# Optimization experiments

Measured on AMD Instinct MI355X. Metric: run time of the kernel, lower is better.

## Reference

```python
import jax, jax.numpy as jnp
import numpy as np
from jax import lax

B, T, N_MELS = 8, 4096, 26
W_FRAMES = 32          # window_frames
CONV_CH, CONV_K = 64, 5
SE_MID = CONV_CH // 4  # se_ratio=4 on feature_dim=conv_channels
H1, H2 = 256, 128      # hidden_dims
SHORT_W, SHORT_H = 8, 128
OUT_CH = 2             # downbeat=True


def setup_inputs() -> dict:
    key = jax.random.key(0)
    ks = jax.random.split(key, 16)
    s = lambda *sh: 1.0 / np.sqrt(sh[0])
    return {
        "x": jax.random.normal(ks[0], (B, T, N_MELS), jnp.float32),
        # conv1d: kernel stored (K, in, out) for NWC/WIO conv
        "conv_w": jax.random.normal(ks[1], (CONV_K, N_MELS, CONV_CH), jnp.float32) * 0.1,
        "conv_b": jax.random.normal(ks[2], (CONV_CH,), jnp.float32) * 0.1,
        # SE on feature_dim=CONV_CH
        "se_w1": jax.random.normal(ks[3], (CONV_CH, SE_MID), jnp.float32) * s(CONV_CH),
        "se_b1": jnp.zeros((SE_MID,), jnp.float32),
        "se_w2": jax.random.normal(ks[4], (SE_MID, CONV_CH), jnp.float32) * s(SE_MID),
        "se_b2": jnp.zeros((CONV_CH,), jnp.float32),
        # long backbone: (W_FRAMES*CONV_CH) -> H1 -> H2
        "w1": jax.random.normal(ks[5], (W_FRAMES * CONV_CH, H1), jnp.float32) * s(W_FRAMES * CONV_CH),
        "b1": jnp.zeros((H1,), jnp.float32),
        "w2": jax.random.normal(ks[6], (H1, H2), jnp.float32) * s(H1),
        "b2": jnp.zeros((H2,), jnp.float32),
        # short backbone: (SHORT_W*CONV_CH) -> SHORT_H
        "sw": jax.random.normal(ks[7], (SHORT_W * CONV_CH, SHORT_H), jnp.float32) * s(SHORT_W * CONV_CH),
        "sb": jnp.zeros((SHORT_H,), jnp.float32),
        # output head: (H2 + SHORT_H) -> OUT_CH
        "wo": jax.random.normal(ks[8], (H2 + SHORT_H, OUT_CH), jnp.float32) * s(H2 + SHORT_H),
        "bo": jnp.zeros((OUT_CH,), jnp.float32),
    }


def reference(x, conv_w, conv_b, se_w1, se_b1, se_w2, se_b2,
              w1, b1, w2, b2, sw, sb, wo, bo):
    batch, time, _ = x.shape
    # 1) causal conv1d over full sequence (left-pad K-1), then ReLU
    xp = jnp.pad(x, ((0, 0), (CONV_K - 1, 0), (0, 0)))
    xc = lax.conv_general_dilated(xp, conv_w, window_strides=(1,),
                                  padding='VALID',
                                  dimension_numbers=('NWC', 'WIO', 'NWC'))
    xc = jax.nn.relu(xc + conv_b)                      # (B, T, F=CONV_CH)
    # 2) causal sliding-window unfold: windows[b,t,w,:] = padded[b, t+w, :]
    x_pad = jnp.pad(xc, ((0, 0), (W_FRAMES - 1, 0), (0, 0)))
    idx = jnp.arange(time)[:, None] + jnp.arange(W_FRAMES)[None, :]
    windows = x_pad[:, idx, :]                          # (B, T, W, F)
    # 3) SE channel attention (pool over window dim)
    s = windows.mean(axis=2)                            # (B, T, F)
    a = jax.nn.sigmoid(jax.nn.relu(s @ se_w1 + se_b1) @ se_w2 + se_b2)
    windows = windows * a[:, :, None, :]
    # 4) long backbone (dropout = identity in eval)
    flat_long = windows.reshape(batch, time, W_FRAMES * CONV_CH)
    h = jax.nn.relu(flat_long @ w1 + b1)
    h = jax.nn.relu(h @ w2 + b2)                        # (B, T, H2)
    # short path: last SHORT_W frames of the same SE-processed window
    flat_short = windows[:, :, -SHORT_W:, :].reshape(batch, time, SHORT_W * CONV_CH)
    h_short = jax.nn.relu(flat_short @ sw + sb)         # (B, T, SHORT_H)
    h = jnp.concatenate([h, h_short], axis=-1)
    # 5) output head
    return jax.nn.sigmoid(h @ wo + bo)                  # (B, T, OUT_CH)
```

## Files before the change

kernel.cpp:

```cpp
#include <hip/hip_runtime.h>

typedef _Float16 half_t;
typedef __attribute__((ext_vector_type(8))) _Float16 h8;
typedef __attribute__((ext_vector_type(2))) _Float16 h2v;
typedef __attribute__((ext_vector_type(4))) float f4;
typedef __attribute__((ext_vector_type(2))) float f2v;

__device__ __forceinline__ half_t to_h(float v) {
    v = fminf(fmaxf(v, -60000.f), 60000.f);
    return (half_t)v;
}

__global__ void pack_k(const float* __restrict__ w1, const float* __restrict__ w2,
                       const float* __restrict__ sw, const float* __restrict__ cw,
                       half_t* __restrict__ wsH) {
    int i = blockIdx.x * 256 + threadIdx.x;
    if (i < 65536) {
        int L = i & 63, nt = (i >> 6) & 15, kk = i >> 10;
        int k0 = kk * 32 + ((L >> 4) << 3), n = (nt << 4) + (L & 15);
        h8 v;
#pragma unroll
        for (int j = 0; j < 8; j++) v[j] = to_h(w1[(k0 + j) * 256 + n]);
        *(h8*)(wsH + ((((kk * 16 + nt) * 64 + L)) << 3)) = v;
    } else if (i < 69632) {
        int o = i - 65536;
        int L = o & 63, nt = (o >> 6) & 7, kk = o >> 9;
        int k0 = kk * 32 + ((L >> 4) << 3), n = (nt << 4) + (L & 15);
        h8 v;
#pragma unroll
        for (int j = 0; j < 8; j++) v[j] = to_h(w2[(k0 + j) * 128 + n]);
        *(h8*)(wsH + 524288 + ((((kk * 8 + nt) * 64 + L)) << 3)) = v;
    } else if (i < 77824) {
        int o = i - 69632;
        int L = o & 63, nt = (o >> 6) & 7, kk = o >> 9;
        int k0 = kk * 32 + ((L >> 4) << 3), n = (nt << 4) + (L & 15);
        h8 v;
#pragma unroll
        for (int j = 0; j < 8; j++) v[j] = to_h(sw[(k0 + j) * 128 + n]);
        *(h8*)(wsH + 557056 + ((((kk * 8 + nt) * 64 + L)) << 3)) = v;
    } else if (i < 86144) {
        int o = i - 77824;
        int c = o & 63, rest = o >> 6;
        int k = rest / 26, ci = rest - k * 26;
        int ip = ci >> 1, r = ci & 1;
        wsH[622592 + ((k * 13 + ip) * 64 + c) * 2 + r] = to_h(cw[o]);
    }
}

#define XCS 72
#define ALS 72
#define Y1S 264
#define SLS 68
#define HLS 20

#define MFMA16(a, b, c) __builtin_amdgcn_mfma_f32_16x16x32_f16(a, b, c, 0, 0, 0)

__global__ __launch_bounds__(512, 4) void beat_main(
    const float* __restrict__ x,
    const float* __restrict__ conv_b,
    const float* __restrict__ se_w1, const float* __restrict__ se_b1,
    const float* __restrict__ se_w2, const float* __restrict__ se_b2,
    const float* __restrict__ b1, const float* __restrict__ b2,
    const float* __restrict__ sb,
    const float* __restrict__ wo, const float* __restrict__ bo,
    const half_t* __restrict__ w1p, const half_t* __restrict__ w2p,
    const half_t* __restrict__ swp, const half_t* __restrict__ cwp,
    float* __restrict__ out) {

    __shared__ __align__(16) char smem[58752];
    half_t* xcL = (half_t*)smem;
    half_t* aL  = (half_t*)(smem + 13696);
    char*   U   = smem + 22912;
    half_t* xLh = (half_t*)U;
    float*  sLf = (float*)U;
    float*  hidL= (float*)(U + 17408);
    half_t* y1L = (half_t*)U;
    float*  woL = (float*)(smem + 56704);

    const int tid = threadIdx.x;
    const int bi = blockIdx.x;
    const int b = bi >> 6;
    const int t0 = (bi & 63) << 6;
    const int lane = tid & 63, wv = tid >> 6;
    const int quad = lane >> 4, rl = lane & 15;
    const int mg = wv >> 2;
    const int ng = wv & 3;
    const int nq = wv & 3;

    if (tid < 256) ((f2v*)woL)[tid] = ((const f2v*)wo)[tid];
    for (int idx = tid; idx < 99 * 13; idx += 512) {
        int fi = idx / 13, ip = idx - fi * 13;
        int tx = t0 - 35 + fi;
        h2v v;
        if (tx >= 0) {
            const float* xp = x + ((size_t)(b * 4096 + tx)) * 26 + 2 * ip;
            v[0] = to_h(xp[0]); v[1] = to_h(xp[1]);
        } else { v[0] = (_Float16)0.f; v[1] = (_Float16)0.f; }
        *(h2v*)(xLh + fi * 28 + 2 * ip) = v;
    }
    __syncthreads();

    {
        int c = tid & 63, f0 = tid >> 6;
        h2v cwr[65];
        const h2v* cwg = (const h2v*)cwp;
#pragma unroll
        for (int p = 0; p < 65; p++) cwr[p] = cwg[p * 64 + c];
        float bias = conv_b[c];
        for (int f = f0; f < 95; f += 8) {
            int t = t0 - 31 + f;
            float r0 = 0.f;
            if (t >= 0) {
                h2v accp; accp[0] = (_Float16)0.f; accp[1] = (_Float16)0.f;
#pragma unroll
                for (int k = 0; k < 5; k++)
#pragma unroll
                    for (int ip = 0; ip < 13; ip++) {
                        h2v xp = *(const h2v*)(xLh + (f + k) * 28 + 2 * ip);
                        accp += xp * cwr[k * 13 + ip];
                    }
                r0 = fmaxf((float)accp[0] + (float)accp[1] + bias, 0.f);
            }
            xcL[f * XCS + c] = to_h(r0);
        }
    }
    __syncthreads();

    {
        int c = tid & 63, mb = tid >> 6;
        float run = 0.f;
#pragma unroll 8
        for (int w = 0; w < 32; w++) run += (float)xcL[(mb + w) * XCS + c];
        sLf[mb * SLS + c] = run * (1.f / 32.f);
        for (int m = mb + 8; m < 64; m += 8) {
#pragma unroll
            for (int d = 0; d < 8; d++) {
                run += (float)xcL[(m + 24 + d) * XCS + c];
                run -= (float)xcL[(m - 8 + d) * XCS + c];
            }
            sLf[m * SLS + c] = run * (1.f / 32.f);
        }
    }
    __syncthreads();

    {
        int m = tid >> 3, hh = (tid & 7) * 2;
        float acc0 = se_b1[hh], acc1 = se_b1[hh + 1];
        for (int c = 0; c < 64; c++) {
            float sv = sLf[m * SLS + c];
            f2v wq = *(const f2v*)(se_w1 + c * 16 + hh);
            acc0 += sv * wq[0]; acc1 += sv * wq[1];
        }
        hidL[m * HLS + hh] = fmaxf(acc0, 0.f);
        hidL[m * HLS + hh + 1] = fmaxf(acc1, 0.f);
    }
    __syncthreads();

    {
        int m = tid >> 3, c0 = (tid & 7) * 8;
        float av[8];
#pragma unroll
        for (int j = 0; j < 8; j++) av[j] = se_b2[c0 + j];
        for (int h = 0; h < 16; h++) {
            float hv = hidL[m * HLS + h];
            const f4* wv4 = (const f4*)(se_w2 + h * 64 + c0);
            f4 wq0 = wv4[0], wq1 = wv4[1];
#pragma unroll
            for (int j = 0; j < 4; j++) { av[j] += hv * wq0[j]; av[4 + j] += hv * wq1[j]; }
        }
#pragma unroll
        for (int j = 0; j < 8; j++) {
            float zz = fminf(fmaxf(av[j], -30.f), 30.f);
            float s = 1.f / (1.f + __expf(-zz));
            aL[m * ALS + c0 + j] = to_h(s);
        }
    }
    __syncthreads();

    {
        f4 acc[2][4];
#pragma unroll
        for (int mt = 0; mt < 2; mt++)
#pragma unroll
            for (int i = 0; i < 4; i++)
#pragma unroll
                for (int r = 0; r < 4; r++) acc[mt][i][r] = 0.f;
        const h8* w1v = (const h8*)w1p;
        const int fb = ng * 4;
        h8 bA[4], bB[4], bC[4], bD[4];
#pragma unroll
        for (int i = 0; i < 4; i++) bA[i] = w1v[(fb + i) * 64 + lane];
#pragma unroll
        for (int i = 0; i < 4; i++) bB[i] = w1v[(16 + fb + i) * 64 + lane];
#pragma unroll 2
        for (int kk = 0; kk < 64; kk += 2) {
            const int k2 = (kk + 2) & 63, k3 = (kk + 3) & 63;
#pragma unroll
            for (int i = 0; i < 4; i++) bC[i] = w1v[(k2 * 16 + fb + i) * 64 + lane];
#pragma unroll
            for (int i = 0; i < 4; i++) bD[i] = w1v[(k3 * 16 + fb + i) * 64 + lane];
            const int wf = kk >> 1;
            {
                const int c0 = quad * 8;
#pragma unroll
                for (int mt = 0; mt < 2; mt++) {
                    int m = mg * 32 + mt * 16 + rl;
                    h8 xv = *(const h8*)(xcL + (m + wf) * XCS + c0);
                    h8 av = *(const h8*)(aL + m * ALS + c0);
                    h8 af = xv * av;
#pragma unroll
                    for (int i = 0; i < 4; i++) acc[mt][i] = MFMA16(af, bA[i], acc[mt][i]);
                }
            }
            {
                const int c0 = 32 + quad * 8;
#pragma unroll
                for (int mt = 0; mt < 2; mt++) {
                    int m = mg * 32 + mt * 16 + rl;
                    h8 xv = *(const h8*)(xcL + (m + wf) * XCS + c0);
                    h8 av = *(const h8*)(aL + m * ALS + c0);
                    h8 af = xv * av;
#pragma unroll
                    for (int i = 0; i < 4; i++) acc[mt][i] = MFMA16(af, bB[i], acc[mt][i]);
                }
            }
#pragma unroll
            for (int i = 0; i < 4; i++) { bA[i] = bC[i]; bB[i] = bD[i]; }
        }
#pragma unroll
        for (int i = 0; i < 4; i++) {
            int n = ng * 64 + i * 16 + rl;
            float bb = b1[n];
#pragma unroll
            for (int mt = 0; mt < 2; mt++)
#pragma unroll
                for (int r = 0; r < 4; r++) {
                    int m = mg * 32 + mt * 16 + quad * 4 + r;
                    y1L[m * Y1S + n] = to_h(fmaxf(acc[mt][i][r] + bb, 0.f));
                }
        }
    }
    __syncthreads();

    f4 acc2[2][2];
#pragma unroll
    for (int mt = 0; mt < 2; mt++)
#pragma unroll
        for (int j = 0; j < 2; j++)
#pragma unroll
            for (int r = 0; r < 4; r++) acc2[mt][j][r] = 0.f;
    {
        const h8* w2v = (const h8*)w2p;
        const int fb2 = nq * 2;
        h8 c0f = w2v[(fb2 + 0) * 64 + lane];
        h8 c1f = w2v[(fb2 + 1) * 64 + lane];
#pragma unroll 2
        for (int kk = 0; kk < 8; kk++) {
            int kn = (kk + 1) & 7;
            h8 n0 = w2v[(kn * 8 + fb2 + 0) * 64 + lane];
            h8 n1 = w2v[(kn * 8 + fb2 + 1) * 64 + lane];
#pragma unroll
            for (int mt = 0; mt < 2; mt++) {
                h8 av = *(const h8*)(y1L + (mg * 32 + mt * 16 + rl) * Y1S + kk * 32 + quad * 8);
                acc2[mt][0] = MFMA16(av, c0f, acc2[mt][0]);
                acc2[mt][1] = MFMA16(av, c1f, acc2[mt][1]);
            }
            c0f = n0; c1f = n1;
        }
    }

    f4 accS[2][2];
#pragma unroll
    for (int mt = 0; mt < 2; mt++)
#pragma unroll
        for (int j = 0; j < 2; j++)
#pragma unroll
            for (int r = 0; r < 4; r++) accS[mt][j][r] = 0.f;
    {
        const h8* swv = (const h8*)swp;
        const int fb2 = nq * 2;
        h8 c0f = swv[(fb2 + 0) * 64 + lane];
        h8 c1f = swv[(fb2 + 1) * 64 + lane];
#pragma unroll 2
        for (int kk = 0; kk < 16; kk++) {
            int kn = (kk + 1) & 15;
            h8 n0 = swv[(kn * 8 + fb2 + 0) * 64 + lane];
            h8 n1 = swv[(kn * 8 + fb2 + 1) * 64 + lane];
            const int wf = 24 + (kk >> 1);
            const int c0 = ((kk & 1) << 5) + quad * 8;
#pragma unroll
            for (int mt = 0; mt < 2; mt++) {
                int m = mg * 32 + mt * 16 + rl;
                h8 xv = *(const h8*)(xcL + (m + wf) * XCS + c0);
                h8 av2 = *(const h8*)(aL + m * ALS + c0);
                h8 af = xv * av2;
                accS[mt][0] = MFMA16(af, c0f, accS[mt][0]);
                accS[mt][1] = MFMA16(af, c1f, accS[mt][1]);
            }
            c0f = n0; c1f = n1;
        }
    }
    __syncthreads();

    {
#pragma unroll
        for (int j = 0; j < 2; j++) {
            int n = nq * 32 + j * 16 + rl;
            float bb2 = b2[n], bbs = sb[n];
#pragma unroll
            for (int mt = 0; mt < 2; mt++)
#pragma unroll
                for (int r = 0; r < 4; r++) {
                    int m = mg * 32 + mt * 16 + quad * 4 + r;
                    y1L[m * Y1S + n]       = to_h(fmaxf(acc2[mt][j][r] + bb2, 0.f));
                    y1L[m * Y1S + 128 + n] = to_h(fmaxf(accS[mt][j][r] + bbs, 0.f));
                }
        }
    }
    __syncthreads();

    if (tid < 128) {
        int m = tid >> 1, o = tid & 1;
        float z = bo[o];
        const half_t* hrow = y1L + m * Y1S;
        for (int nb = 0; nb < 32; nb++) {
            h8 hv = *(const h8*)(hrow + nb * 8);
#pragma unroll
            for (int j = 0; j < 8; j++)
                z += (float)hv[j] * woL[(nb * 8 + j) * 2 + o];
        }
        z = fminf(fmaxf(z, -30.f), 30.f);
        float sg = 1.f / (1.f + __expf(-z));
        out[((size_t)(b * 4096 + t0 + m)) * 2 + o] = sg;
    }
}

extern "C" void kernel_launch(void* const* d_in, const int* in_sizes, int n_in,
                              void* d_out, int out_size, void* d_ws, size_t ws_size,
                              hipStream_t stream) {
    const float* x      = (const float*)d_in[0];
    const float* conv_w = (const float*)d_in[1];
    const float* conv_b = (const float*)d_in[2];
    const float* se_w1  = (const float*)d_in[3];
    const float* se_b1  = (const float*)d_in[4];
    const float* se_w2  = (const float*)d_in[5];
    const float* se_b2  = (const float*)d_in[6];
    const float* w1     = (const float*)d_in[7];
    const float* b1     = (const float*)d_in[8];
    const float* w2     = (const float*)d_in[9];
    const float* b2     = (const float*)d_in[10];
    const float* sw     = (const float*)d_in[11];
    const float* sb     = (const float*)d_in[12];
    const float* wo     = (const float*)d_in[13];
    const float* bo     = (const float*)d_in[14];
    half_t* wsH = (half_t*)d_ws;

    hipLaunchKernelGGL(pack_k, dim3(337), dim3(256), 0, stream, w1, w2, sw, conv_w, wsH);
    hipLaunchKernelGGL(beat_main, dim3(512), dim3(512), 0, stream,
                       x, conv_b, se_w1, se_b1, se_w2, se_b2, b1, b2, sb, wo, bo,
                       wsH, wsH + 524288, wsH + 557056, wsH + 622592,
                       (float*)d_out);
}
```

Measured before the change: 152.7 us.

## Split conv and SE attention into prep kernel, stream results into GEMM kernel

Moves the causal conv, sliding mean and SE attention out of the GEMM kernel into a prep kernel that also packs weights. The prep kernel handles 128-frame tiles, so the 31-frame halo conv is recomputed less often. It writes conv output and attention gates to global workspace in fp16. The GEMM kernel reloads these, keeps the gates in registers and uses less shared memory, which may raise occupancy. The cost is an extra global round trip for the intermediates and a serial dependency between the two launches.

```diff
diff --git a/kernel.cpp b/kernel.cpp
--- a/kernel.cpp
+++ b/kernel.cpp
@@ -11,71 +11,178 @@
     return (half_t)v;
 }
 
-__global__ void pack_k(const float* __restrict__ w1, const float* __restrict__ w2,
-                       const float* __restrict__ sw, const float* __restrict__ cw,
-                       half_t* __restrict__ wsH) {
-    int i = blockIdx.x * 256 + threadIdx.x;
-    if (i < 65536) {
-        int L = i & 63, nt = (i >> 6) & 15, kk = i >> 10;
-        int k0 = kk * 32 + ((L >> 4) << 3), n = (nt << 4) + (L & 15);
-        h8 v;
-#pragma unroll
-        for (int j = 0; j < 8; j++) v[j] = to_h(w1[(k0 + j) * 256 + n]);
-        *(h8*)(wsH + ((((kk * 16 + nt) * 64 + L)) << 3)) = v;
-    } else if (i < 69632) {
-        int o = i - 65536;
-        int L = o & 63, nt = (o >> 6) & 7, kk = o >> 9;
-        int k0 = kk * 32 + ((L >> 4) << 3), n = (nt << 4) + (L & 15);
-        h8 v;
-#pragma unroll
-        for (int j = 0; j < 8; j++) v[j] = to_h(w2[(k0 + j) * 128 + n]);
-        *(h8*)(wsH + 524288 + ((((kk * 8 + nt) * 64 + L)) << 3)) = v;
-    } else if (i < 77824) {
-        int o = i - 69632;
-        int L = o & 63, nt = (o >> 6) & 7, kk = o >> 9;
-        int k0 = kk * 32 + ((L >> 4) << 3), n = (nt << 4) + (L & 15);
-        h8 v;
-#pragma unroll
-        for (int j = 0; j < 8; j++) v[j] = to_h(sw[(k0 + j) * 128 + n]);
-        *(h8*)(wsH + 557056 + ((((kk * 8 + nt) * 64 + L)) << 3)) = v;
-    } else if (i < 86144) {
-        int o = i - 77824;
-        int c = o & 63, rest = o >> 6;
-        int k = rest / 26, ci = rest - k * 26;
-        int ip = ci >> 1, r = ci & 1;
-        wsH[622592 + ((k * 13 + ip) * 64 + c) * 2 + r] = to_h(cw[o]);
-    }
-}
-
-#define XCS 72
-#define ALS 72
-#define Y1S 264
-#define SLS 68
-#define HLS 20
-
-#define MFMA16(a, b, c) __builtin_amdgcn_mfma_f32_16x16x32_f16(a, b, c, 0, 0, 0)
-
-__global__ __launch_bounds__(512, 4) void beat_main(
-    const float* __restrict__ x,
+#define W2P_OFF 524288
+#define SWP_OFF 557056
+#define XCG_OFF 622592
+#define AG_OFF  2719744
+
+__global__ __launch_bounds__(512) void beat_prep(
+    const float* __restrict__ x, const float* __restrict__ conv_w,
     const float* __restrict__ conv_b,
     const float* __restrict__ se_w1, const float* __restrict__ se_b1,
     const float* __restrict__ se_w2, const float* __restrict__ se_b2,
+    const float* __restrict__ w1, const float* __restrict__ w2,
+    const float* __restrict__ sw,
+    half_t* __restrict__ wsH) {
+
+    const int bi = blockIdx.x;
+    const int tid = threadIdx.x;
+
+    if (bi >= 256) {
+        int j = (bi - 256) * 512 + tid;
+        if (j < 65536) {
+            int L = j & 63, nt = (j >> 6) & 15, kk = j >> 10;
+            int k0 = kk * 32 + ((L >> 4) << 3), n = (nt << 4) + (L & 15);
+            h8 v;
+#pragma unroll
+            for (int q = 0; q < 8; q++) v[q] = to_h(w1[(k0 + q) * 256 + n]);
+            *(h8*)(wsH + (((kk * 16 + nt) * 64 + L) << 3)) = v;
+        } else if (j < 69632) {
+            int o = j - 65536;
+            int L = o & 63, nt = (o >> 6) & 7, kk = o >> 9;
+            int k0 = kk * 32 + ((L >> 4) << 3), n = (nt << 4) + (L & 15);
+            h8 v;
+#pragma unroll
+            for (int q = 0; q < 8; q++) v[q] = to_h(w2[(k0 + q) * 128 + n]);
+            *(h8*)(wsH + W2P_OFF + (((kk * 8 + nt) * 64 + L) << 3)) = v;
+        } else {
+            int o = j - 69632;
+            int L = o & 63, nt = (o >> 6) & 7, kk = o >> 9;
+            int k0 = kk * 32 + ((L >> 4) << 3), n = (nt << 4) + (L & 15);
+            h8 v;
+#pragma unroll
+            for (int q = 0; q < 8; q++) v[q] = to_h(sw[(k0 + q) * 128 + n]);
+            *(h8*)(wsH + SWP_OFF + (((kk * 8 + nt) * 64 + L) << 3)) = v;
+        }
+        return;
+    }
+
+    __shared__ __align__(16) char smem[54560];
+    half_t* xLh  = (half_t*)smem;
+    half_t* xcA  = (half_t*)(smem + 9136);
+    float*  sLf  = (float*)(smem + 32032);
+    float*  hidL = (float*)(smem + 49440);
+    half_t* xc_g = wsH + XCG_OFF;
+    half_t* a_g  = wsH + AG_OFF;
+
+    const int b = bi >> 5;
+    const int t0a = (bi & 31) << 7;
+
+    for (int idx = tid; idx < 163 * 13; idx += 512) {
+        int fi = idx / 13, ip = idx - fi * 13;
+        int tx = t0a - 35 + fi;
+        h2v v;
+        if (tx >= 0) {
+            const float* xp = x + ((size_t)(b * 4096 + tx)) * 26 + 2 * ip;
+            v[0] = to_h(xp[0]); v[1] = to_h(xp[1]);
+        } else { v[0] = (_Float16)0.f; v[1] = (_Float16)0.f; }
+        *(h2v*)(xLh + fi * 28 + 2 * ip) = v;
+    }
+    __syncthreads();
+
+    {
+        int c = tid & 63, f0 = tid >> 6;
+        h2v cwr[65];
+#pragma unroll
+        for (int p = 0; p < 65; p++) {
+            int k = p / 13, ip = p - k * 13;
+            cwr[p][0] = to_h(conv_w[(k * 26 + 2 * ip) * 64 + c]);
+            cwr[p][1] = to_h(conv_w[(k * 26 + 2 * ip + 1) * 64 + c]);
+        }
+        float bias = conv_b[c];
+        for (int f = f0; f < 159; f += 8) {
+            int t = t0a + f - 31;
+            float r0 = 0.f;
+            if (t >= 0) {
+                h2v accp; accp[0] = (_Float16)0.f; accp[1] = (_Float16)0.f;
+#pragma unroll
+                for (int k = 0; k < 5; k++)
+#pragma unroll
+                    for (int ip = 0; ip < 13; ip++) {
+                        h2v xp = *(const h2v*)(xLh + (f + k) * 28 + 2 * ip);
+                        accp += xp * cwr[k * 13 + ip];
+                    }
+                r0 = fmaxf((float)accp[0] + (float)accp[1] + bias, 0.f);
+            }
+            half_t hv = to_h(r0);
+            xcA[f * 72 + c] = hv;
+            if (f >= 31) xc_g[((size_t)(b * 4096 + t)) * 64 + c] = hv;
+        }
+    }
+    __syncthreads();
+
+    for (int sub = 0; sub < 2; sub++) {
+        const int base = sub * 64;
+        {
+            int c = tid & 63, mb = tid >> 6;
+            float run = 0.f;
+#pragma unroll 8
+            for (int w = 0; w < 32; w++) run += (float)xcA[(base + mb + w) * 72 + c];
+            sLf[mb * 68 + c] = run * (1.f / 32.f);
+            for (int m = mb + 8; m < 64; m += 8) {
+#pragma unroll
+                for (int d = 0; d < 8; d++) {
+                    run += (float)xcA[(base + m + 24 + d) * 72 + c];
+                    run -= (float)xcA[(base + m - 8 + d) * 72 + c];
+                }
+                sLf[m * 68 + c] = run * (1.f / 32.f);
+            }
+        }
+        __syncthreads();
+        {
+            int m = tid >> 3, hh = (tid & 7) * 2;
+            float acc0 = se_b1[hh], acc1 = se_b1[hh + 1];
+            for (int c = 0; c < 64; c++) {
+                float sv = sLf[m * 68 + c];
+                f2v wq = *(const f2v*)(se_w1 + c * 16 + hh);
+                acc0 += sv * wq[0]; acc1 += sv * wq[1];
+            }
+            hidL[m * 20 + hh] = fmaxf(acc0, 0.f);
+            hidL[m * 20 + hh + 1] = fmaxf(acc1, 0.f);
+        }
+        __syncthreads();
+        {
+            int m = tid >> 3, c0 = (tid & 7) * 8;
+            float av[8];
+#pragma unroll
+            for (int q = 0; q < 8; q++) av[q] = se_b2[c0 + q];
+            for (int h = 0; h < 16; h++) {
+                float hv = hidL[m * 20 + h];
+                const f4* wv4 = (const f4*)(se_w2 + h * 64 + c0);
+                f4 wq0 = wv4[0], wq1 = wv4[1];
+#pragma unroll
+                for (int q = 0; q < 4; q++) { av[q] += hv * wq0[q]; av[4 + q] += hv * wq1[q]; }
+            }
+            h8 ov;
+#pragma unroll
+            for (int q = 0; q < 8; q++) {
+                float zz = fminf(fmaxf(av[q], -30.f), 30.f);
+                ov[q] = to_h(1.f / (1.f + __expf(-zz)));
+            }
+            *(h8*)(a_g + ((size_t)(b * 4096 + t0a + base + m)) * 64 + c0) = ov;
+        }
+        __syncthreads();
+    }
+}
+
+#define XCS 72
+#define Y1S 264
+
+#define MFMA16(a, b, c) __builtin_amdgcn_mfma_f32_16x16x32_f16(a, b, c, 0, 0, 0)
+
+__global__ __launch_bounds__(512, 4) void beat_gemm(
     const float* __restrict__ b1, const float* __restrict__ b2,
     const float* __restrict__ sb,
     const float* __restrict__ wo, const float* __restrict__ bo,
     const half_t* __restrict__ w1p, const half_t* __restrict__ w2p,
-    const half_t* __restrict__ swp, const half_t* __restrict__ cwp,
+    const half_t* __restrict__ swp,
+    const half_t* __restrict__ xc_g, const half_t* __restrict__ a_g,
     float* __restrict__ out) {
 
-    __shared__ __align__(16) char smem[58752];
+    __shared__ __align__(16) char smem[49536];
     half_t* xcL = (half_t*)smem;
-    half_t* aL  = (half_t*)(smem + 13696);
-    char*   U   = smem + 22912;
-    half_t* xLh = (half_t*)U;
-    float*  sLf = (float*)U;
-    float*  hidL= (float*)(U + 17408);
-    half_t* y1L = (half_t*)U;
-    float*  woL = (float*)(smem + 56704);
+    half_t* y1L = (half_t*)(smem + 13696);
+    float*  woL = (float*)(smem + 47488);
 
     const int tid = threadIdx.x;
     const int bi = blockIdx.x;
@@ -88,93 +195,23 @@
     const int nq = wv & 3;
 
     if (tid < 256) ((f2v*)woL)[tid] = ((const f2v*)wo)[tid];
-    for (int idx = tid; idx < 99 * 13; idx += 512) {
-        int fi = idx / 13, ip = idx - fi * 13;
-        int tx = t0 - 35 + fi;
-        h2v v;
-        if (tx >= 0) {
-            const float* xp = x + ((size_t)(b * 4096 + tx)) * 26 + 2 * ip;
-            v[0] = to_h(xp[0]); v[1] = to_h(xp[1]);
-        } else { v[0] = (_Float16)0.f; v[1] = (_Float16)0.f; }
-        *(h2v*)(xLh + fi * 28 + 2 * ip) = v;
-    }
-    __syncthreads();
-
-    {
-        int c = tid & 63, f0 = tid >> 6;
-        h2v cwr[65];
-        const h2v* cwg = (const h2v*)cwp;
-#pragma unroll
-        for (int p = 0; p < 65; p++) cwr[p] = cwg[p * 64 + c];
-        float bias = conv_b[c];
-        for (int f = f0; f < 95; f += 8) {
-            int t = t0 - 31 + f;
-            float r0 = 0.f;
-            if (t >= 0) {
-                h2v accp; accp[0] = (_Float16)0.f; accp[1] = (_Float16)0.f;
-#pragma unroll
-                for (int k = 0; k < 5; k++)
-#pragma unroll
-                    for (int ip = 0; ip < 13; ip++) {
-                        h2v xp = *(const h2v*)(xLh + (f + k) * 28 + 2 * ip);
-                        accp += xp * cwr[k * 13 + ip];
-                    }
-                r0 = fmaxf((float)accp[0] + (float)accp[1] + bias, 0.f);
-            }
-            xcL[f * XCS + c] = to_h(r0);
-        }
-    }
-    __syncthreads();
-
-    {
-        int c = tid & 63, mb = tid >> 6;
-        float run = 0.f;
-#pragma unroll 8
-        for (int w = 0; w < 32; w++) run += (float)xcL[(mb + w) * XCS + c];
-        sLf[mb * SLS + c] = run * (1.f / 32.f);
-        for (int m = mb + 8; m < 64; m += 8) {
-#pragma unroll
-            for (int d = 0; d < 8; d++) {
-                run += (float)xcL[(m + 24 + d) * XCS + c];
-                run -= (float)xcL[(m - 8 + d) * XCS + c];
-            }
-            sLf[m * SLS + c] = run * (1.f / 32.f);
-        }
-    }
-    __syncthreads();
-
-    {
-        int m = tid >> 3, hh = (tid & 7) * 2;
-        float acc0 = se_b1[hh], acc1 = se_b1[hh + 1];
-        for (int c = 0; c < 64; c++) {
-            float sv = sLf[m * SLS + c];
-            f2v wq = *(const f2v*)(se_w1 + c * 16 + hh);
-            acc0 += sv * wq[0]; acc1 += sv * wq[1];
-        }
-        hidL[m * HLS + hh] = fmaxf(acc0, 0.f);
-        hidL[m * HLS + hh + 1] = fmaxf(acc1, 0.f);
-    }
-    __syncthreads();
-
-    {
-        int m = tid >> 3, c0 = (tid & 7) * 8;
-        float av[8];
-#pragma unroll
-        for (int j = 0; j < 8; j++) av[j] = se_b2[c0 + j];
-        for (int h = 0; h < 16; h++) {
-            float hv = hidL[m * HLS + h];
-            const f4* wv4 = (const f4*)(se_w2 + h * 64 + c0);
-            f4 wq0 = wv4[0], wq1 = wv4[1];
-#pragma unroll
-            for (int j = 0; j < 4; j++) { av[j] += hv * wq0[j]; av[4 + j] += hv * wq1[j]; }
-        }
-#pragma unroll
-        for (int j = 0; j < 8; j++) {
-            float zz = fminf(fmaxf(av[j], -30.f), 30.f);
-            float s = 1.f / (1.f + __expf(-zz));
-            aL[m * ALS + c0 + j] = to_h(s);
-        }
-    }
+    for (int idx = tid; idx < 95 * 8; idx += 512) {
+        int fi = idx >> 3, jp = idx & 7;
+        int t = t0 - 31 + fi;
+        h8 v;
+        if (t >= 0) v = *(const h8*)(xc_g + ((size_t)(b * 4096 + t)) * 64 + jp * 8);
+        else {
+#pragma unroll
+            for (int q = 0; q < 8; q++) v[q] = (_Float16)0.f;
+        }
+        *(h8*)(xcL + fi * XCS + jp * 8) = v;
+    }
+    h8 avr[2][2];
+#pragma unroll
+    for (int mt = 0; mt < 2; mt++)
+#pragma unroll
+        for (int p = 0; p < 2; p++)
+            avr[mt][p] = *(const h8*)(a_g + ((size_t)(b * 4096 + t0 + mg * 32 + mt * 16 + rl)) * 64 + p * 32 + quad * 8);
     __syncthreads();
 
     {
@@ -206,8 +243,7 @@
                 for (int mt = 0; mt < 2; mt++) {
                     int m = mg * 32 + mt * 16 + rl;
                     h8 xv = *(const h8*)(xcL + (m + wf) * XCS + c0);
-                    h8 av = *(const h8*)(aL + m * ALS + c0);
-                    h8 af = xv * av;
+                    h8 af = xv * avr[mt][0];
 #pragma unroll
                     for (int i = 0; i < 4; i++) acc[mt][i] = MFMA16(af, bA[i], acc[mt][i]);
                 }
@@ -218,8 +254,7 @@
                 for (int mt = 0; mt < 2; mt++) {
                     int m = mg * 32 + mt * 16 + rl;
                     h8 xv = *(const h8*)(xcL + (m + wf) * XCS + c0);
-                    h8 av = *(const h8*)(aL + m * ALS + c0);
-                    h8 af = xv * av;
+                    h8 af = xv * avr[mt][1];
 #pragma unroll
                     for (int i = 0; i < 4; i++) acc[mt][i] = MFMA16(af, bB[i], acc[mt][i]);
                 }
@@ -292,8 +327,7 @@
             for (int mt = 0; mt < 2; mt++) {
                 int m = mg * 32 + mt * 16 + rl;
                 h8 xv = *(const h8*)(xcL + (m + wf) * XCS + c0);
-                h8 av2 = *(const h8*)(aL + m * ALS + c0);
-                h8 af = xv * av2;
+                h8 af = xv * avr[mt][kk & 1];
                 accS[mt][0] = MFMA16(af, c0f, accS[mt][0]);
                 accS[mt][1] = MFMA16(af, c1f, accS[mt][1]);
             }
@@ -326,8 +360,8 @@
         for (int nb = 0; nb < 32; nb++) {
             h8 hv = *(const h8*)(hrow + nb * 8);
 #pragma unroll
-            for (int j = 0; j < 8; j++)
-                z += (float)hv[j] * woL[(nb * 8 + j) * 2 + o];
+            for (int q = 0; q < 8; q++)
+                z += (float)hv[q] * woL[(nb * 8 + q) * 2 + o];
         }
         z = fminf(fmaxf(z, -30.f), 30.f);
         float sg = 1.f / (1.f + __expf(-z));
@@ -355,9 +389,11 @@
     const float* bo     = (const float*)d_in[14];
     half_t* wsH = (half_t*)d_ws;
 
-    hipLaunchKernelGGL(pack_k, dim3(337), dim3(256), 0, stream, w1, w2, sw, conv_w, wsH);
-    hipLaunchKernelGGL(beat_main, dim3(512), dim3(512), 0, stream,
-                       x, conv_b, se_w1, se_b1, se_w2, se_b2, b1, b2, sb, wo, bo,
-                       wsH, wsH + 524288, wsH + 557056, wsH + 622592,
+    hipLaunchKernelGGL(beat_prep, dim3(408), dim3(512), 0, stream,
+                       x, conv_w, conv_b, se_w1, se_b1, se_w2, se_b2, w1, w2, sw, wsH);
+    hipLaunchKernelGGL(beat_gemm, dim3(512), dim3(512), 0, stream,
+                       b1, b2, sb, wo, bo,
+                       wsH, wsH + W2P_OFF, wsH + SWP_OFF,
+                       wsH + XCG_OFF, wsH + AG_OFF,
                        (float*)d_out);
 }
```

New measurement: 182.5 us. +19.5%, slower.

## Remap warps to cover all 64 rows with narrower column slices, cache SE scales

Applied to the files above, without the earlier changes.

Each of the 8 wavefronts now handles all 64 time rows and a narrower slice of output columns in the W1, W2 and short-path GEMMs, where before it used a 2x4 row/column split. Each wavefront therefore loads half as many W1 fragments (2 instead of 4 per k-step), which cuts global weight traffic per block. The SE attention fragments are loaded into registers once and reused across all k-steps instead of being reread from LDS every iteration. In exchange each wavefront reads twice as many activation rows from LDS per k-step and holds more accumulator and attention registers.

```diff
diff --git a/kernel.cpp b/kernel.cpp
--- a/kernel.cpp
+++ b/kernel.cpp
@@ -83,9 +83,6 @@
     const int t0 = (bi & 63) << 6;
     const int lane = tid & 63, wv = tid >> 6;
     const int quad = lane >> 4, rl = lane & 15;
-    const int mg = wv >> 2;
-    const int ng = wv & 3;
-    const int nq = wv & 3;
 
     if (tid < 256) ((f2v*)woL)[tid] = ((const f2v*)wo)[tid];
     for (int idx = tid; idx < 99 * 13; idx += 512) {
@@ -177,145 +174,134 @@
     }
     __syncthreads();
 
-    {
-        f4 acc[2][4];
-#pragma unroll
-        for (int mt = 0; mt < 2; mt++)
-#pragma unroll
-            for (int i = 0; i < 4; i++)
+    h8 avr[4][2];
+#pragma unroll
+    for (int mt = 0; mt < 4; mt++)
+#pragma unroll
+        for (int p = 0; p < 2; p++)
+            avr[mt][p] = *(const h8*)(aL + (mt * 16 + rl) * ALS + p * 32 + quad * 8);
+
+    {
+        f4 acc[4][2];
+#pragma unroll
+        for (int mt = 0; mt < 4; mt++)
+#pragma unroll
+            for (int i = 0; i < 2; i++)
 #pragma unroll
                 for (int r = 0; r < 4; r++) acc[mt][i][r] = 0.f;
         const h8* w1v = (const h8*)w1p;
-        const int fb = ng * 4;
-        h8 bA[4], bB[4], bC[4], bD[4];
-#pragma unroll
-        for (int i = 0; i < 4; i++) bA[i] = w1v[(fb + i) * 64 + lane];
-#pragma unroll
-        for (int i = 0; i < 4; i++) bB[i] = w1v[(16 + fb + i) * 64 + lane];
+        const int fb = wv * 2;
+        h8 bA[2], bB[2], bC[2], bD[2];
+#pragma unroll
+        for (int i = 0; i < 2; i++) bA[i] = w1v[(fb + i) * 64 + lane];
+#pragma unroll
+        for (int i = 0; i < 2; i++) bB[i] = w1v[(16 + fb + i) * 64 + lane];
 #pragma unroll 2
         for (int kk = 0; kk < 64; kk += 2) {
             const int k2 = (kk + 2) & 63, k3 = (kk + 3) & 63;
 #pragma unroll
-            for (int i = 0; i < 4; i++) bC[i] = w1v[(k2 * 16 + fb + i) * 64 + lane];
-#pragma unroll
-            for (int i = 0; i < 4; i++) bD[i] = w1v[(k3 * 16 + fb + i) * 64 + lane];
+            for (int i = 0; i < 2; i++) bC[i] = w1v[(k2 * 16 + fb + i) * 64 + lane];
+#pragma unroll
+            for (int i = 0; i < 2; i++) bD[i] = w1v[(k3 * 16 + fb + i) * 64 + lane];
             const int wf = kk >> 1;
             {
                 const int c0 = quad * 8;
 #pragma unroll
-                for (int mt = 0; mt < 2; mt++) {
-                    int m = mg * 32 + mt * 16 + rl;
+                for (int mt = 0; mt < 4; mt++) {
+                    int m = mt * 16 + rl;
                     h8 xv = *(const h8*)(xcL + (m + wf) * XCS + c0);
-                    h8 av = *(const h8*)(aL + m * ALS + c0);
-                    h8 af = xv * av;
-#pragma unroll
-                    for (int i = 0; i < 4; i++) acc[mt][i] = MFMA16(af, bA[i], acc[mt][i]);
+                    h8 af = xv * avr[mt][0];
+                    acc[mt][0] = MFMA16(af, bA[0], acc[mt][0]);
+                    acc[mt][1] = MFMA16(af, bA[1], acc[mt][1]);
                 }
             }
             {
                 const int c0 = 32 + quad * 8;
 #pragma unroll
-                for (int mt = 0; mt < 2; mt++) {
-                    int m = mg * 32 + mt * 16 + rl;
+                for (int mt = 0; mt < 4; mt++) {
+                    int m = mt * 16 + rl;
                     h8 xv = *(const h8*)(xcL + (m + wf) * XCS + c0);
-                    h8 av = *(const h8*)(aL + m * ALS + c0);
-                    h8 af = xv * av;
-#pragma unroll
-                    for (int i = 0; i < 4; i++) acc[mt][i] = MFMA16(af, bB[i], acc[mt][i]);
+                    h8 af = xv * avr[mt][1];
+                    acc[mt][0] = MFMA16(af, bB[0], acc[mt][0]);
+                    acc[mt][1] = MFMA16(af, bB[1], acc[mt][1]);
                 }
             }
 #pragma unroll
-            for (int i = 0; i < 4; i++) { bA[i] = bC[i]; bB[i] = bD[i]; }
-        }
-#pragma unroll
-        for (int i = 0; i < 4; i++) {
-            int n = ng * 64 + i * 16 + rl;
+            for (int i = 0; i < 2; i++) { bA[i] = bC[i]; bB[i] = bD[i]; }
+        }
+#pragma unroll
+        for (int i = 0; i < 2; i++) {
+            int n = wv * 32 + i * 16 + rl;
             float bb = b1[n];
 #pragma unroll
-            for (int mt = 0; mt < 2; mt++)
+            for (int mt = 0; mt < 4; mt++)
 #pragma unroll
                 for (int r = 0; r < 4; r++) {
-                    int m = mg * 32 + mt * 16 + quad * 4 + r;
+                    int m = mt * 16 + quad * 4 + r;
                     y1L[m * Y1S + n] = to_h(fmaxf(acc[mt][i][r] + bb, 0.f));
                 }
         }
     }
     __syncthreads();
 
-    f4 acc2[2][2];
-#pragma unroll
-    for (int mt = 0; mt < 2; mt++)
-#pragma unroll
-        for (int j = 0; j < 2; j++)
-#pragma unroll
-            for (int r = 0; r < 4; r++) acc2[mt][j][r] = 0.f;
+    f4 acc2[4];
+#pragma unroll
+    for (int mt = 0; mt < 4; mt++)
+#pragma unroll
+        for (int r = 0; r < 4; r++) acc2[mt][r] = 0.f;
     {
         const h8* w2v = (const h8*)w2p;
-        const int fb2 = nq * 2;
-        h8 c0f = w2v[(fb2 + 0) * 64 + lane];
-        h8 c1f = w2v[(fb2 + 1) * 64 + lane];
+        h8 cf = w2v[wv * 64 + lane];
 #pragma unroll 2
         for (int kk = 0; kk < 8; kk++) {
             int kn = (kk + 1) & 7;
-            h8 n0 = w2v[(kn * 8 + fb2 + 0) * 64 + lane];
-            h8 n1 = w2v[(kn * 8 + fb2 + 1) * 64 + lane];
-#pragma unroll
-            for (int mt = 0; mt < 2; mt++) {
-                h8 av = *(const h8*)(y1L + (mg * 32 + mt * 16 + rl) * Y1S + kk * 32 + quad * 8);
-                acc2[mt][0] = MFMA16(av, c0f, acc2[mt][0]);
-                acc2[mt][1] = MFMA16(av, c1f, acc2[mt][1]);
-            }
-            c0f = n0; c1f = n1;
-        }
-    }
-
-    f4 accS[2][2];
-#pragma unroll
-    for (int mt = 0; mt < 2; mt++)
-#pragma unroll
-        for (int j = 0; j < 2; j++)
-#pragma unroll
-            for (int r = 0; r < 4; r++) accS[mt][j][r] = 0.f;
+            h8 nf = w2v[(kn * 8 + wv) * 64 + lane];
+#pragma unroll
+            for (int mt = 0; mt < 4; mt++) {
+                h8 av = *(const h8*)(y1L + (mt * 16 + rl) * Y1S + kk * 32 + quad * 8);
+                acc2[mt] = MFMA16(av, cf, acc2[mt]);
+            }
+            cf = nf;
+        }
+    }
+
+    f4 accS[4];
+#pragma unroll
+    for (int mt = 0; mt < 4; mt++)
+#pragma unroll
+        for (int r = 0; r < 4; r++) accS[mt][r] = 0.f;
     {
         const h8* swv = (const h8*)swp;
-        const int fb2 = nq * 2;
-        h8 c0f = swv[(fb2 + 0) * 64 + lane];
-        h8 c1f = swv[(fb2 + 1) * 64 + lane];
+        h8 cf = swv[wv * 64 + lane];
 #pragma unroll 2
         for (int kk = 0; kk < 16; kk++) {
             int kn = (kk + 1) & 15;
-            h8 n0 = swv[(kn * 8 + fb2 + 0) * 64 + lane];
-            h8 n1 = swv[(kn * 8 + fb2 + 1) * 64 + lane];
+            h8 nf = swv[(kn * 8 + wv) * 64 + lane];
             const int wf = 24 + (kk >> 1);
             const int c0 = ((kk & 1) << 5) + quad * 8;
 #pragma unroll
-            for (int mt = 0; mt < 2; mt++) {
-                int m = mg * 32 + mt * 16 + rl;
+            for (int mt = 0; mt < 4; mt++) {
+                int m = mt * 16 + rl;
                 h8 xv = *(const h8*)(xcL + (m + wf) * XCS + c0);
-                h8 av2 = *(const h8*)(aL + m * ALS + c0);
-                h8 af = xv * av2;
-                accS[mt][0] = MFMA16(af, c0f, accS[mt][0]);
-                accS[mt][1] = MFMA16(af, c1f, accS[mt][1]);
-            }
-            c0f = n0; c1f = n1;
-        }
-    }
-    __syncthreads();
-
-    {
-#pragma unroll
-        for (int j = 0; j < 2; j++) {
-            int n = nq * 32 + j * 16 + rl;
-            float bb2 = b2[n], bbs = sb[n];
-#pragma unroll
-            for (int mt = 0; mt < 2; mt++)
-#pragma unroll
-                for (int r = 0; r < 4; r++) {
-                    int m = mg * 32 + mt * 16 + quad * 4 + r;
-                    y1L[m * Y1S + n]       = to_h(fmaxf(acc2[mt][j][r] + bb2, 0.f));
-                    y1L[m * Y1S + 128 + n] = to_h(fmaxf(accS[mt][j][r] + bbs, 0.f));
-                }
-        }
+                h8 af = xv * avr[mt][kk & 1];
+                accS[mt] = MFMA16(af, cf, accS[mt]);
+            }
+            cf = nf;
+        }
+    }
+    __syncthreads();
+
+    {
+        int n = wv * 16 + rl;
+        float bb2 = b2[n], bbs = sb[n];
+#pragma unroll
+        for (int mt = 0; mt < 4; mt++)
+#pragma unroll
+            for (int r = 0; r < 4; r++) {
+                int m = mt * 16 + quad * 4 + r;
+                y1L[m * Y1S + n]       = to_h(fmaxf(acc2[mt][r] + bb2, 0.f));
+                y1L[m * Y1S + 128 + n] = to_h(fmaxf(accS[mt][r] + bbs, 0.f));
+            }
     }
     __syncthreads();
 
@@ -326,8 +312,8 @@
         for (int nb = 0; nb < 32; nb++) {
             h8 hv = *(const h8*)(hrow + nb * 8);
 #pragma unroll
-            for (int j = 0; j < 8; j++)
-                z += (float)hv[j] * woL[(nb * 8 + j) * 2 + o];
+            for (int q = 0; q < 8; q++)
+                z += (float)hv[q] * woL[(nb * 8 + q) * 2 + o];
         }
         z = fminf(fmaxf(z, -30.f), 30.f);
         float sg = 1.f / (1.f + __expf(-z));
```

After: 147.5 us. -3.4%, faster.
